# Kernel optimization log

Measured on AMD Instinct MI355X. Metric: run time of the kernel, lower is better.

Reference implementation:

```python
import jax, jax.numpy as jnp
import numpy as np


def setup_inputs() -> dict:
    key = jax.random.key(0)
    ks = jax.random.split(key, 6)
    B, F, C = 2048, 512, 64
    t_feat = jax.random.normal(ks[0], (B, F), dtype=jnp.float32)
    f_feat = jax.random.normal(ks[1], (B, F), dtype=jnp.float32)
    # proj Linear(F*F -> C); scale like torch default init (~1/sqrt(fan_in))
    W_proj = jax.random.normal(ks[2], (C, F * F), dtype=jnp.float32) / np.sqrt(F * F)
    b_proj = jnp.zeros((C,), dtype=jnp.float32)
    W1 = jax.random.normal(ks[3], (32, C), dtype=jnp.float32) / np.sqrt(C)
    b1 = jnp.zeros((32,), dtype=jnp.float32)
    W2 = jax.random.normal(ks[4], (1, 32), dtype=jnp.float32) / np.sqrt(32)
    b2 = jnp.zeros((1,), dtype=jnp.float32)
    return {"t_feat": t_feat, "f_feat": f_feat, "W_proj": W_proj, "b_proj": b_proj,
            "W1": W1, "b1": b1, "W2": W2, "b2": b2}


def reference(t_feat, f_feat, W_proj, b_proj, W1, b1, W2, b2):
    B, F = t_feat.shape
    C = W_proj.shape[0]
    # corr[b,i,j] = t[b,i] * f[b,j]; proj = corr_flat @ W_proj.T + b_proj.
    # Equivalent bilinear form computed WITHOUT materializing the (B,F,F) outer product:
    Wr = W_proj.reshape(C, F, F)            # W_proj[c, i*F + j] -> Wr[c,i,j]
    tmp = jnp.einsum('bi,cij->bcj', t_feat, Wr)   # (B, C, F)
    proj = jnp.einsum('bcj,bj->bc', tmp, f_feat) + b_proj  # (B, C)
    h = jax.nn.relu(proj)
    # GRL is identity in forward
    h2 = jax.nn.relu(h @ W1.T + b1)          # (B, 32)
    logit = h2 @ W2.T + b2                   # (B, 1)
    return logit
```

## Files before the change

kernel.cpp:

```cpp
#include <hip/hip_runtime.h>
#include <hip/hip_bf16.h>
#include <stdint.h>

#define BATCH 2048
#define FDIM 512
#define CDIM 64

typedef unsigned short ushort_t;
typedef __attribute__((ext_vector_type(8))) short short8;
typedef __attribute__((ext_vector_type(4))) float f32x4;

__device__ __forceinline__ ushort_t f2bf(float x) {
    union { float f; uint32_t u; } v; v.f = x;
    uint32_t u = v.u;
    uint32_t r = u + 0x7FFFu + ((u >> 16) & 1u);
    return (ushort_t)(r >> 16);
}

__global__ void convert_kernel(const float* __restrict__ src, ushort_t* __restrict__ dst) {
    int idx = blockIdx.x * 256 + threadIdx.x;
    float4 v0 = ((const float4*)src)[idx * 2];
    float4 v1 = ((const float4*)src)[idx * 2 + 1];
    ushort_t p[8] = { f2bf(v0.x), f2bf(v0.y), f2bf(v0.z), f2bf(v0.w),
                      f2bf(v1.x), f2bf(v1.y), f2bf(v1.z), f2bf(v1.w) };
    *(uint4*)&dst[idx * 8] = *(uint4*)p;
}

#define AS3(p) ((__attribute__((address_space(3))) void*)(p))
#define AS1(p) ((const __attribute__((address_space(1))) void*)(p))

__launch_bounds__(256, 2)
__global__ void gemm_fused_kernel(const ushort_t* __restrict__ f16,
                                  const ushort_t* __restrict__ Wb,
                                  const float* __restrict__ t_feat,
                                  float* __restrict__ part) {
    __shared__ ushort_t As[128 * 64];
    __shared__ ushort_t Bs[128 * 64];
    __shared__ float scratch[256];

    const int tid  = threadIdx.x;
    const int wave = tid >> 6;
    const int lane = tid & 63;
    const int l15  = lane & 15;
    const int lg   = lane >> 4;

    const int g   = blockIdx.x + (blockIdx.y << 4);
    const int xcd = g & 7;
    const int s   = g >> 3;
    const int b0  = (s & 15) << 7;
    const int n0  = (xcd * 32 + (s >> 4)) << 7;

    const int m_base = (wave >> 1) * 64;
    const int nh     = wave & 1;
    const int n_base = nh * 64;

    f32x4 acc[4][4];
    #pragma unroll
    for (int mi = 0; mi < 4; mi++)
        #pragma unroll
        for (int ni = 0; ni < 4; ni++)
            acc[mi][ni] = (f32x4){0.f, 0.f, 0.f, 0.f};

    const ushort_t* srcA[4];
    const ushort_t* srcB[4];
    #pragma unroll
    for (int q = 0; q < 4; q++) {
        int seg  = wave * 4 + q;
        int prow = seg * 8 + (lane >> 3);
        int pch  = lane & 7;
        int gch  = pch ^ (prow & 7);
        srcA[q] = f16 + (size_t)(b0 + prow) * FDIM + gch * 8;
        int grow = (prow & 64) | ((prow & 15) << 2) | ((prow >> 4) & 3);
        srcB[q] = Wb + (size_t)(n0 + grow) * FDIM + gch * 8;
    }

    for (int k0 = 0; k0 < FDIM; k0 += 64) {
        #pragma unroll
        for (int q = 0; q < 4; q++) {
            int seg = wave * 4 + q;
            __builtin_amdgcn_global_load_lds(AS1(srcA[q] + k0), AS3(&As[seg * 512]), 16, 0, 0);
            __builtin_amdgcn_global_load_lds(AS1(srcB[q] + k0), AS3(&Bs[seg * 512]), 16, 0, 0);
        }
        __syncthreads();

        #pragma unroll
        for (int w = 0; w < 2; w++) {
            short8 a[4], b[4];
            #pragma unroll
            for (int mi = 0; mi < 4; mi++) {
                int r  = m_base + mi * 16 + l15;
                int pc = (w * 4 + lg) ^ (r & 7);
                a[mi] = *(const short8*)&As[r * 64 + pc * 8];
            }
            #pragma unroll
            for (int ni = 0; ni < 4; ni++) {
                int q2 = n_base + ni * 16 + l15;
                int pc = (w * 4 + lg) ^ (q2 & 7);
                b[ni] = *(const short8*)&Bs[q2 * 64 + pc * 8];
            }
            #pragma unroll
            for (int mi = 0; mi < 4; mi++)
                #pragma unroll
                for (int ni = 0; ni < 4; ni++)
                    acc[mi][ni] = __builtin_amdgcn_mfma_f32_16x16x32_bf16(a[mi], b[ni], acc[mi][ni], 0, 0, 0);
        }
        __syncthreads();
    }

    const int c  = n0 >> 9;
    const int iq = (n0 >> 7) & 3;
    const int i_base = (n0 & 511) + n_base + l15 * 4;

    #pragma unroll
    for (int mi = 0; mi < 4; mi++) {
        #pragma unroll
        for (int r = 0; r < 4; r++) {
            int b_idx = b0 + m_base + mi * 16 + lg * 4 + r;
            const float4 tv = *(const float4*)&t_feat[(size_t)b_idx * FDIM + i_base];
            float sv = acc[mi][0][r] * tv.x + acc[mi][1][r] * tv.y
                     + acc[mi][2][r] * tv.z + acc[mi][3][r] * tv.w;
            sv += __shfl_xor(sv, 1, 64);
            sv += __shfl_xor(sv, 2, 64);
            sv += __shfl_xor(sv, 4, 64);
            sv += __shfl_xor(sv, 8, 64);
            if (l15 == 0)
                scratch[(m_base + mi * 16 + lg * 4 + r) * 2 + nh] = sv;
        }
    }
    __syncthreads();
    if (tid < 128) {
        float v = scratch[tid * 2] + scratch[tid * 2 + 1];
        part[(((size_t)(b0 + tid)) * 64 + c) * 4 + iq] = v;
    }
}

__global__ void mlp_kernel(const float* __restrict__ part,
                           const float* __restrict__ b_proj,
                           const float* __restrict__ W1, const float* __restrict__ b1,
                           const float* __restrict__ W2, const float* __restrict__ b2,
                           float* __restrict__ out) {
    __shared__ float h[8][64];
    const int tid = threadIdx.x;
    const int bl  = tid >> 5;
    const int o   = tid & 31;
    const int b   = blockIdx.x * 8 + bl;

    #pragma unroll
    for (int c = o; c < 64; c += 32) {
        float4 v = *(const float4*)&part[(((size_t)b * 64 + c)) * 4];
        float sv = v.x + v.y + v.z + v.w + b_proj[c];
        h[bl][c] = sv > 0.f ? sv : 0.f;
    }
    __syncthreads();

    float sv = b1[o];
    #pragma unroll
    for (int c = 0; c < 64; c++) sv += h[bl][c] * W1[o * 64 + c];
    float v = (sv > 0.f ? sv : 0.f) * W2[o];
    v += __shfl_xor(v, 1, 32);
    v += __shfl_xor(v, 2, 32);
    v += __shfl_xor(v, 4, 32);
    v += __shfl_xor(v, 8, 32);
    v += __shfl_xor(v, 16, 32);
    if (o == 0) out[b] = v + b2[0];
}

extern "C" void kernel_launch(void* const* d_in, const int* in_sizes, int n_in,
                              void* d_out, int out_size, void* d_ws, size_t ws_size,
                              hipStream_t stream) {
    const float* t_feat = (const float*)d_in[0];
    const float* f_feat = (const float*)d_in[1];
    const float* W_proj = (const float*)d_in[2];
    const float* b_proj = (const float*)d_in[3];
    const float* W1     = (const float*)d_in[4];
    const float* b1     = (const float*)d_in[5];
    const float* W2     = (const float*)d_in[6];
    const float* b2     = (const float*)d_in[7];
    float* out = (float*)d_out;

    uint8_t* ws = (uint8_t*)d_ws;
    ushort_t* Wb   = (ushort_t*)(ws);
    ushort_t* f16  = (ushort_t*)(ws + 33554432);
    float*    part = (float*)(ws + 33554432 + 2097152);

    convert_kernel<<<dim3((CDIM * FDIM * FDIM) / 2048), dim3(256), 0, stream>>>(W_proj, Wb);
    convert_kernel<<<dim3((BATCH * FDIM) / 2048), dim3(256), 0, stream>>>(f_feat, f16);

    gemm_fused_kernel<<<dim3(BATCH / 128, (CDIM * FDIM) / 128), dim3(256), 0, stream>>>(
        f16, Wb, t_feat, part);

    mlp_kernel<<<dim3(BATCH / 8), dim3(256), 0, stream>>>(part, b_proj, W1, b1, W2, b2, out);
}
```

Baseline: 217.1 us.

## Fuse W_proj fp32-to-bf16 conversion into GEMM tile loads

Drops the separate pass that converted the 64MB fp32 W_proj to bf16. The GEMM now streams fp32 W tiles straight into LDS and converts them to bf16 in registers before the MFMA. The K tile is halved to 32 and the A tile layout and swizzle are reworked to fit. This removes a 64MB read plus a 32MB write and a kernel launch, but the GEMM now reads twice as many weight bytes and spends VALU time on conversion inside the inner loop.

```diff
diff --git a/kernel.cpp b/kernel.cpp
--- a/kernel.cpp
+++ b/kernel.cpp
@@ -31,11 +31,11 @@
 
 __launch_bounds__(256, 2)
 __global__ void gemm_fused_kernel(const ushort_t* __restrict__ f16,
-                                  const ushort_t* __restrict__ Wb,
+                                  const float* __restrict__ W,
                                   const float* __restrict__ t_feat,
                                   float* __restrict__ part) {
-    __shared__ ushort_t As[128 * 64];
-    __shared__ ushort_t Bs[128 * 64];
+    __shared__ ushort_t As[128 * 32];
+    __shared__ float    Bs[128 * 32];
     __shared__ float scratch[256];
 
     const int tid  = threadIdx.x;
@@ -61,49 +61,59 @@
         for (int ni = 0; ni < 4; ni++)
             acc[mi][ni] = (f32x4){0.f, 0.f, 0.f, 0.f};
 
-    const ushort_t* srcA[4];
-    const ushort_t* srcB[4];
+    const int pA   = tid >> 2;
+    const int cphA = tid & 3;
+    const int cgA  = cphA ^ ((pA >> 1) & 3);
+    const ushort_t* srcA0 = f16 + (size_t)(b0 + pA) * FDIM + cgA * 8;
+    const ushort_t* srcA1 = srcA0 + (size_t)64 * FDIM;
+
+    const float* srcB[4];
     #pragma unroll
     for (int q = 0; q < 4; q++) {
         int seg  = wave * 4 + q;
         int prow = seg * 8 + (lane >> 3);
         int pch  = lane & 7;
         int gch  = pch ^ (prow & 7);
-        srcA[q] = f16 + (size_t)(b0 + prow) * FDIM + gch * 8;
         int grow = (prow & 64) | ((prow & 15) << 2) | ((prow >> 4) & 3);
-        srcB[q] = Wb + (size_t)(n0 + grow) * FDIM + gch * 8;
-    }
-
-    for (int k0 = 0; k0 < FDIM; k0 += 64) {
+        srcB[q]  = W + (size_t)(n0 + grow) * FDIM + gch * 4;
+    }
+
+    for (int k0 = 0; k0 < FDIM; k0 += 32) {
+        __builtin_amdgcn_global_load_lds(AS1(srcA0 + k0), AS3(&As[0 * 2048 + wave * 512]), 16, 0, 0);
+        __builtin_amdgcn_global_load_lds(AS1(srcA1 + k0), AS3(&As[1 * 2048 + wave * 512]), 16, 0, 0);
         #pragma unroll
         for (int q = 0; q < 4; q++) {
             int seg = wave * 4 + q;
-            __builtin_amdgcn_global_load_lds(AS1(srcA[q] + k0), AS3(&As[seg * 512]), 16, 0, 0);
-            __builtin_amdgcn_global_load_lds(AS1(srcB[q] + k0), AS3(&Bs[seg * 512]), 16, 0, 0);
+            __builtin_amdgcn_global_load_lds(AS1(srcB[q] + k0), AS3(&Bs[seg * 256]), 16, 0, 0);
         }
         __syncthreads();
 
-        #pragma unroll
-        for (int w = 0; w < 2; w++) {
-            short8 a[4], b[4];
+        short8 a[4], b[4];
+        #pragma unroll
+        for (int mi = 0; mi < 4; mi++) {
+            int r = m_base + mi * 16 + l15;
+            a[mi] = *(const short8*)&As[r * 32 + (lg ^ ((r >> 1) & 3)) * 8];
+        }
+        #pragma unroll
+        for (int ni = 0; ni < 4; ni++) {
+            int q2 = n_base + ni * 16 + l15;
+            int h  = q2 & 7;
+            float4 v0 = *(const float4*)&Bs[q2 * 32 + (((2 * lg) ^ h) * 4)];
+            float4 v1 = *(const float4*)&Bs[q2 * 32 + (((2 * lg + 1) ^ h) * 4)];
+            union { __hip_bfloat162 h2[4]; short8 s; } pk;
+            pk.h2[0] = __float22bfloat162_rn(make_float2(v0.x, v0.y));
+            pk.h2[1] = __float22bfloat162_rn(make_float2(v0.z, v0.w));
+            pk.h2[2] = __float22bfloat162_rn(make_float2(v1.x, v1.y));
+            pk.h2[3] = __float22bfloat162_rn(make_float2(v1.z, v1.w));
+            b[ni] = pk.s;
+        }
+
+        #pragma unroll
+        for (int mi = 0; mi < 4; mi++)
             #pragma unroll
-            for (int mi = 0; mi < 4; mi++) {
-                int r  = m_base + mi * 16 + l15;
-                int pc = (w * 4 + lg) ^ (r & 7);
-                a[mi] = *(const short8*)&As[r * 64 + pc * 8];
-            }
-            #pragma unroll
-            for (int ni = 0; ni < 4; ni++) {
-                int q2 = n_base + ni * 16 + l15;
-                int pc = (w * 4 + lg) ^ (q2 & 7);
-                b[ni] = *(const short8*)&Bs[q2 * 64 + pc * 8];
-            }
-            #pragma unroll
-            for (int mi = 0; mi < 4; mi++)
-                #pragma unroll
-                for (int ni = 0; ni < 4; ni++)
-                    acc[mi][ni] = __builtin_amdgcn_mfma_f32_16x16x32_bf16(a[mi], b[ni], acc[mi][ni], 0, 0, 0);
-        }
+            for (int ni = 0; ni < 4; ni++)
+                acc[mi][ni] = __builtin_amdgcn_mfma_f32_16x16x32_bf16(a[mi], b[ni], acc[mi][ni], 0, 0, 0);
+
         __syncthreads();
     }
 
@@ -179,15 +189,13 @@
     float* out = (float*)d_out;
 
     uint8_t* ws = (uint8_t*)d_ws;
-    ushort_t* Wb   = (ushort_t*)(ws);
-    ushort_t* f16  = (ushort_t*)(ws + 33554432);
-    float*    part = (float*)(ws + 33554432 + 2097152);
-
-    convert_kernel<<<dim3((CDIM * FDIM * FDIM) / 2048), dim3(256), 0, stream>>>(W_proj, Wb);
+    ushort_t* f16  = (ushort_t*)(ws);
+    float*    part = (float*)(ws + 2097152);
+
     convert_kernel<<<dim3((BATCH * FDIM) / 2048), dim3(256), 0, stream>>>(f_feat, f16);
 
     gemm_fused_kernel<<<dim3(BATCH / 128, (CDIM * FDIM) / 128), dim3(256), 0, stream>>>(
-        f16, Wb, t_feat, part);
+        f16, W_proj, t_feat, part);
 
     mlp_kernel<<<dim3(BATCH / 8), dim3(256), 0, stream>>>(part, b_proj, W1, b1, W2, b2, out);
 }
```

Result: slower. 240.1 us (+10.6%).

## Halve GEMM K-tile, drop XCD block remap, and convert t_feat to bf16

Applied to the files above, without the earlier changes.

The GEMM main loop now stages 32-wide K tiles instead of 64-wide, with a new 4-chunk swizzle and a different load-to-LDS address mapping. This halves LDS use per block but doubles the number of barriers and iterations. The XCD-aware block index remapping is removed in favour of plain blockIdx tiling, which may hurt L2 reuse of W across chiplets. t_feat is also converted to bf16 in a combined conversion kernel and read as bf16 in the epilogue, which cuts epilogue bandwidth at some cost in precision.

```diff
diff --git a/kernel.cpp b/kernel.cpp
--- a/kernel.cpp
+++ b/kernel.cpp
@@ -16,9 +16,25 @@
     uint32_t r = u + 0x7FFFu + ((u >> 16) & 1u);
     return (ushort_t)(r >> 16);
 }
+__device__ __forceinline__ float bf2f(ushort_t u) {
+    union { float f; uint32_t v; } x; x.v = ((uint32_t)u) << 16; return x.f;
+}
 
 __global__ void convert_kernel(const float* __restrict__ src, ushort_t* __restrict__ dst) {
     int idx = blockIdx.x * 256 + threadIdx.x;
+    float4 v0 = ((const float4*)src)[idx * 2];
+    float4 v1 = ((const float4*)src)[idx * 2 + 1];
+    ushort_t p[8] = { f2bf(v0.x), f2bf(v0.y), f2bf(v0.z), f2bf(v0.w),
+                      f2bf(v1.x), f2bf(v1.y), f2bf(v1.z), f2bf(v1.w) };
+    *(uint4*)&dst[idx * 8] = *(uint4*)p;
+}
+
+__global__ void convert_ft_kernel(const float* __restrict__ f, ushort_t* __restrict__ f16,
+                                  const float* __restrict__ t, ushort_t* __restrict__ t16) {
+    int blk = blockIdx.x;
+    const float* src = (blk < 512) ? f : t;
+    ushort_t* dst    = (blk < 512) ? f16 : t16;
+    int idx = (blk & 511) * 256 + threadIdx.x;
     float4 v0 = ((const float4*)src)[idx * 2];
     float4 v1 = ((const float4*)src)[idx * 2 + 1];
     ushort_t p[8] = { f2bf(v0.x), f2bf(v0.y), f2bf(v0.z), f2bf(v0.w),
@@ -32,10 +48,10 @@
 __launch_bounds__(256, 2)
 __global__ void gemm_fused_kernel(const ushort_t* __restrict__ f16,
                                   const ushort_t* __restrict__ Wb,
-                                  const float* __restrict__ t_feat,
+                                  const ushort_t* __restrict__ t16,
                                   float* __restrict__ part) {
-    __shared__ ushort_t As[128 * 64];
-    __shared__ ushort_t Bs[128 * 64];
+    __shared__ ushort_t As[128 * 32];
+    __shared__ ushort_t Bs[128 * 32];
     __shared__ float scratch[256];
 
     const int tid  = threadIdx.x;
@@ -44,11 +60,8 @@
     const int l15  = lane & 15;
     const int lg   = lane >> 4;
 
-    const int g   = blockIdx.x + (blockIdx.y << 4);
-    const int xcd = g & 7;
-    const int s   = g >> 3;
-    const int b0  = (s & 15) << 7;
-    const int n0  = (xcd * 32 + (s >> 4)) << 7;
+    const int b0 = blockIdx.x * 128;
+    const int n0 = blockIdx.y * 128;
 
     const int m_base = (wave >> 1) * 64;
     const int nh     = wave & 1;
@@ -61,49 +74,41 @@
         for (int ni = 0; ni < 4; ni++)
             acc[mi][ni] = (f32x4){0.f, 0.f, 0.f, 0.f};
 
-    const ushort_t* srcA[4];
-    const ushort_t* srcB[4];
-    #pragma unroll
-    for (int q = 0; q < 4; q++) {
-        int seg  = wave * 4 + q;
-        int prow = seg * 8 + (lane >> 3);
-        int pch  = lane & 7;
-        int gch  = pch ^ (prow & 7);
-        srcA[q] = f16 + (size_t)(b0 + prow) * FDIM + gch * 8;
-        int grow = (prow & 64) | ((prow & 15) << 2) | ((prow >> 4) & 3);
-        srcB[q] = Wb + (size_t)(n0 + grow) * FDIM + gch * 8;
-    }
+    const int p    = tid >> 2;
+    const int cph  = tid & 3;
+    const int cg   = cph ^ ((p >> 1) & 3);
+    const int nrot = ((p & 15) << 2) | (p >> 4);
 
-    for (int k0 = 0; k0 < FDIM; k0 += 64) {
-        #pragma unroll
-        for (int q = 0; q < 4; q++) {
-            int seg = wave * 4 + q;
-            __builtin_amdgcn_global_load_lds(AS1(srcA[q] + k0), AS3(&As[seg * 512]), 16, 0, 0);
-            __builtin_amdgcn_global_load_lds(AS1(srcB[q] + k0), AS3(&Bs[seg * 512]), 16, 0, 0);
-        }
+    const ushort_t* gA0 = f16 + (size_t)(b0 + p) * FDIM + cg * 8;
+    const ushort_t* gA1 = f16 + (size_t)(b0 + 64 + p) * FDIM + cg * 8;
+    const ushort_t* gB0 = Wb + (size_t)(n0 + nrot) * FDIM + cg * 8;
+    const ushort_t* gB1 = Wb + (size_t)(n0 + 64 + nrot) * FDIM + cg * 8;
+
+    for (int k0 = 0; k0 < FDIM; k0 += 32) {
+        __builtin_amdgcn_global_load_lds(AS1(gA0 + k0), AS3(&As[0 * 2048 + wave * 512]), 16, 0, 0);
+        __builtin_amdgcn_global_load_lds(AS1(gA1 + k0), AS3(&As[1 * 2048 + wave * 512]), 16, 0, 0);
+        __builtin_amdgcn_global_load_lds(AS1(gB0 + k0), AS3(&Bs[0 * 2048 + wave * 512]), 16, 0, 0);
+        __builtin_amdgcn_global_load_lds(AS1(gB1 + k0), AS3(&Bs[1 * 2048 + wave * 512]), 16, 0, 0);
         __syncthreads();
 
+        short8 a[4], b[4];
         #pragma unroll
-        for (int w = 0; w < 2; w++) {
-            short8 a[4], b[4];
+        for (int mi = 0; mi < 4; mi++) {
+            int r = m_base + mi * 16 + l15;
+            a[mi] = *(const short8*)&As[r * 32 + (lg ^ ((r >> 1) & 3)) * 8];
+        }
+        #pragma unroll
+        for (int ni = 0; ni < 4; ni++) {
+            int q = n_base + ni * 16 + l15;
+            b[ni] = *(const short8*)&Bs[q * 32 + (lg ^ ((q >> 1) & 3)) * 8];
+        }
+
+        #pragma unroll
+        for (int mi = 0; mi < 4; mi++)
             #pragma unroll
-            for (int mi = 0; mi < 4; mi++) {
-                int r  = m_base + mi * 16 + l15;
-                int pc = (w * 4 + lg) ^ (r & 7);
-                a[mi] = *(const short8*)&As[r * 64 + pc * 8];
-            }
-            #pragma unroll
-            for (int ni = 0; ni < 4; ni++) {
-                int q2 = n_base + ni * 16 + l15;
-                int pc = (w * 4 + lg) ^ (q2 & 7);
-                b[ni] = *(const short8*)&Bs[q2 * 64 + pc * 8];
-            }
-            #pragma unroll
-            for (int mi = 0; mi < 4; mi++)
-                #pragma unroll
-                for (int ni = 0; ni < 4; ni++)
-                    acc[mi][ni] = __builtin_amdgcn_mfma_f32_16x16x32_bf16(a[mi], b[ni], acc[mi][ni], 0, 0, 0);
-        }
+            for (int ni = 0; ni < 4; ni++)
+                acc[mi][ni] = __builtin_amdgcn_mfma_f32_16x16x32_bf16(a[mi], b[ni], acc[mi][ni], 0, 0, 0);
+
         __syncthreads();
     }
 
@@ -116,9 +121,9 @@
         #pragma unroll
         for (int r = 0; r < 4; r++) {
             int b_idx = b0 + m_base + mi * 16 + lg * 4 + r;
-            const float4 tv = *(const float4*)&t_feat[(size_t)b_idx * FDIM + i_base];
-            float sv = acc[mi][0][r] * tv.x + acc[mi][1][r] * tv.y
-                     + acc[mi][2][r] * tv.z + acc[mi][3][r] * tv.w;
+            ushort4 tv = *(const ushort4*)&t16[(size_t)b_idx * FDIM + i_base];
+            float sv = acc[mi][0][r] * bf2f(tv.x) + acc[mi][1][r] * bf2f(tv.y)
+                     + acc[mi][2][r] * bf2f(tv.z) + acc[mi][3][r] * bf2f(tv.w);
             sv += __shfl_xor(sv, 1, 64);
             sv += __shfl_xor(sv, 2, 64);
             sv += __shfl_xor(sv, 4, 64);
@@ -181,13 +186,14 @@
     uint8_t* ws = (uint8_t*)d_ws;
     ushort_t* Wb   = (ushort_t*)(ws);
     ushort_t* f16  = (ushort_t*)(ws + 33554432);
-    float*    part = (float*)(ws + 33554432 + 2097152);
+    ushort_t* t16  = (ushort_t*)(ws + 33554432 + 2097152);
+    float*    part = (float*)(ws + 33554432 + 2 * 2097152);
 
     convert_kernel<<<dim3((CDIM * FDIM * FDIM) / 2048), dim3(256), 0, stream>>>(W_proj, Wb);
-    convert_kernel<<<dim3((BATCH * FDIM) / 2048), dim3(256), 0, stream>>>(f_feat, f16);
+    convert_ft_kernel<<<dim3(1024), dim3(256), 0, stream>>>(f_feat, f16, t_feat, t16);
 
     gemm_fused_kernel<<<dim3(BATCH / 128, (CDIM * FDIM) / 128), dim3(256), 0, stream>>>(
-        f16, Wb, t_feat, part);
+        f16, Wb, t16, part);
 
     mlp_kernel<<<dim3(BATCH / 8), dim3(256), 0, stream>>>(part, b_proj, W1, b1, W2, b2, out);
 }
```

Result: no change. 213.9 us (-1.5%).
